# Kernel optimization log

Measured on AMD Instinct MI355X. Metric: run time of the kernel, lower is better.

The kernel has to match this reference:

```python
import jax, jax.numpy as jnp
import numpy as np

BOS, EOS, MAX_STEPS = 1, 2, 50
VOCAB, EMBD, HID, CTX, SEQ = 50257, 512, 1024, 1024, 50


def setup_inputs() -> dict:
    key = jax.random.key(0)
    ks = jax.random.split(key, 13)
    s = 0.05
    return {
        "seq_enc_states": jax.random.normal(ks[0], (SEQ, 1, CTX), jnp.float32),
        "seq_enc_hidden": jax.random.normal(ks[1], (1, CTX), jnp.float32),
        "E": jax.random.normal(ks[2], (VOCAB, EMBD), jnp.float32) * s,
        "W_init": jax.random.normal(ks[3], (HID, CTX), jnp.float32) * s,
        "b_init": jax.random.normal(ks[4], (HID,), jnp.float32) * s,
        "Wa": jax.random.normal(ks[5], (CTX, HID), jnp.float32) * s,
        "ba": jax.random.normal(ks[6], (CTX,), jnp.float32) * s,
        "W_ih": jax.random.normal(ks[7], (3 * HID, EMBD + CTX), jnp.float32) * s,
        "W_hh": jax.random.normal(ks[8], (3 * HID, HID), jnp.float32) * s,
        "b_ih": jax.random.normal(ks[9], (3 * HID,), jnp.float32) * s,
        "b_hh": jax.random.normal(ks[10], (3 * HID,), jnp.float32) * s,
        "Wv": jax.random.normal(ks[11], (VOCAB, HID), jnp.float32) * s,
        "bv": jax.random.normal(ks[12], (VOCAB,), jnp.float32) * s,
    }


def _gru_cell(x, h, W_ih, W_hh, b_ih, b_hh):
    # torch.nn.GRUCell math
    gi = x @ W_ih.T + b_ih  # (1, 3H)
    gh = h @ W_hh.T + b_hh  # (1, 3H)
    i_r, i_z, i_n = jnp.split(gi, 3, axis=-1)
    h_r, h_z, h_n = jnp.split(gh, 3, axis=-1)
    r = jax.nn.sigmoid(i_r + h_r)
    z = jax.nn.sigmoid(i_z + h_z)
    n = jnp.tanh(i_n + r * h_n)
    return (1.0 - z) * n + z * h


def reference(seq_enc_states, seq_enc_hidden, E, W_init, b_init, Wa, ba,
              W_ih, W_hh, b_ih, b_hh, Wv, bv):
    enc = seq_enc_states[:, 0, :]                       # (S, CTX)
    h0 = seq_enc_hidden.reshape(1, -1) @ W_init.T + b_init  # (1, H)
    emb0 = E[BOS][None, :]                              # (1, EMBD)

    def step(carry, _):
        h, emb, done = carry
        # dot-product attention over the 50 encoder positions
        ph = h @ Wa.T + ba                              # (1, CTX)
        attn = jax.nn.softmax(ph @ enc.T, axis=-1)      # (1, S)
        ctx = attn @ enc                                # (1, CTX)
        x = jnp.concatenate([emb, ctx], axis=-1)        # (1, EMBD+CTX)
        h_new = _gru_cell(x, h, W_ih, W_hh, b_ih, b_hh)
        logp = jax.nn.log_softmax(h_new @ Wv.T + bv, axis=-1)  # (1, V)
        idx = jnp.argmax(logp[0])
        valid = jnp.logical_not(done)
        is_eos = idx == EOS
        emit_idx = jnp.where(valid & jnp.logical_not(is_eos), idx, -1).astype(jnp.int32)
        logp_out = jnp.where(valid, logp[0], 0.0)
        new_emb = jnp.where((valid & jnp.logical_not(is_eos))[..., None], E[idx][None, :], emb)
        new_h = jnp.where(valid, h_new, h)
        new_done = done | is_eos
        return (new_h, new_emb, new_done), (emit_idx, logp_out, valid)

    init = (h0, emb0, jnp.array(False))
    _, (indices, logps, valid) = jax.lax.scan(step, init, None, length=MAX_STEPS)
    # indices: (50,) int32, -1 where past eos / eos itself (not appended in original)
    return indices, logps, valid
```

## Files before the change

kernel.cpp:

```cpp
#include <hip/hip_runtime.h>
#include <hip/hip_fp16.h>
#include <cmath>

#define VOCABSZ 50257
#define EMBD 512
#define HIDD 1024
#define CTXD 1024
#define SEQL 50
#define NSTEPS 50
#define BOS_ID 1
#define EOS_ID 2

#define NTHR 256
#define NB_GH 768
#define NB_GI 768
#define NB_WR 64
#define NB_PRE (NB_GH + NB_GI + NB_WR)
#define NB_LOG 832
#define NW_LOG (NB_LOG * 4)

#define OFF_M      0
#define OFF_T      51200
#define OFF_H      51264
#define OFF_CTX    53312
#define OFF_GI     54336
#define OFF_GH     57408
#define OFF_L      60480
#define OFF_STATS  110784
#define OFF_STATE  117440
#define OFF_WVH    117568

__device__ __forceinline__ float wred_sum(float v) {
#pragma unroll
  for (int o = 32; o > 0; o >>= 1) v += __shfl_xor(v, o, 64);
  return v;
}

__device__ __forceinline__ float dot4(float4 a, float4 b) {
  return a.x * b.x + a.y * b.y + a.z * b.z + a.w * b.w;
}

__device__ __forceinline__ float wdot1024(const float* __restrict__ row, int lane,
                                          float4 b0, float4 b1, float4 b2, float4 b3) {
  const float4* r = (const float4*)row;
  float acc = dot4(r[lane], b0) + dot4(r[lane + 64], b1) +
              dot4(r[lane + 128], b2) + dot4(r[lane + 192], b3);
  return wred_sum(acc);
}

__device__ __forceinline__ bool beats(float v, int i, float v0, int i0) {
  return v > v0 || (v == v0 && i < i0);
}

__device__ __forceinline__ void top2_merge(float& v1, int& i1, float& v2, int& i2,
                                           float w1, int j1, float w2, int j2) {
  if (beats(w1, j1, v1, i1)) {
    float nv2; int ni2;
    if (beats(v1, i1, w2, j2)) { nv2 = v1; ni2 = i1; } else { nv2 = w2; ni2 = j2; }
    v1 = w1; i1 = j1; v2 = nv2; i2 = ni2;
  } else if (beats(w1, j1, v2, i2)) {
    v2 = w1; i2 = j1;
  }
}

__device__ __forceinline__ float acc8(uint4 a, const float* b) {
  const __half2* h = reinterpret_cast<const __half2*>(&a);
  float2 f0 = __half22float2(h[0]);
  float2 f1 = __half22float2(h[1]);
  float2 f2 = __half22float2(h[2]);
  float2 f3 = __half22float2(h[3]);
  return f0.x * b[0] + f0.y * b[1] + f1.x * b[2] + f1.y * b[3] +
         f2.x * b[4] + f2.y * b[5] + f3.x * b[6] + f3.y * b[7];
}

__global__ void __launch_bounds__(NTHR)
k_cvt(const float4* __restrict__ src, uint2* __restrict__ dst, int n4) {
  int i = blockIdx.x * NTHR + threadIdx.x;
  const int stride = gridDim.x * NTHR;
  for (; i < n4; i += stride) {
    float4 v = src[i];
    __half2 a = __floats2half2_rn(v.x, v.y);
    __half2 b = __floats2half2_rn(v.z, v.w);
    uint2 u;
    u.x = *reinterpret_cast<unsigned*>(&a);
    u.y = *reinterpret_cast<unsigned*>(&b);
    dst[i] = u;
  }
}

__global__ void __launch_bounds__(1024)
k0_matM(float* __restrict__ ws, const float* __restrict__ enc,
        const float* __restrict__ Wa) {
  const int kc = blockIdx.x;
  const int jg = blockIdx.y;
  const int tid = threadIdx.x;
  const int w = tid >> 6, lane = tid & 63;
  const int jw = w & 3, q = w >> 2;
  const int j = jg * 4 + jw;
  const int k = kc * 64 + lane;
  __shared__ float s_red[16][64];
  float acc0 = 0.f, acc1 = 0.f, acc2 = 0.f, acc3 = 0.f;
  if (j < SEQL) {
    const float4* e4 = (const float4*)(enc + (size_t)j * CTXD);
    const float* Wc = Wa + k;
    for (int c4 = q * 64; c4 < q * 64 + 64; ++c4) {
      float4 e = e4[c4];
      const float* wp = Wc + (size_t)(c4 * 4) * HIDD;
      acc0 += e.x * wp[0];
      acc1 += e.y * wp[HIDD];
      acc2 += e.z * wp[2 * HIDD];
      acc3 += e.w * wp[3 * HIDD];
    }
  }
  s_red[w][lane] = acc0 + acc1 + acc2 + acc3;
  __syncthreads();
  if (q == 0 && j < SEQL) {
    float v = s_red[jw][lane] + s_red[4 + jw][lane] +
              s_red[8 + jw][lane] + s_red[12 + jw][lane];
    ws[OFF_M + (size_t)j * HIDD + k] = v;
  }
}

__global__ void __launch_bounds__(NTHR)
k0_init(float* __restrict__ ws, const float* __restrict__ enc,
        const float* __restrict__ hid0, const float* __restrict__ Winit,
        const float* __restrict__ binit, const float* __restrict__ ba) {
  const int blk = blockIdx.x, tid = threadIdx.x;
  const int wave = tid >> 6, lane = tid & 63;
  if (blk == 0) {
    const float4* b4 = (const float4*)ba;
    float4 b0 = b4[lane], b1 = b4[lane + 64], b2 = b4[lane + 128], b3 = b4[lane + 192];
    for (int j = wave; j < SEQL; j += 4) {
      float v = wdot1024(enc + (size_t)j * CTXD, lane, b0, b1, b2, b3);
      if (lane == 0) ws[OFF_T + j] = v;
    }
    if (tid == 0) {
      int* st_emb = (int*)(ws + OFF_STATE);
      st_emb[0] = BOS_ID;
      st_emb[64] = 0;
    }
  } else {
    const float4* h4 = (const float4*)hid0;
    float4 b0 = h4[lane], b1 = h4[lane + 64], b2 = h4[lane + 128], b3 = h4[lane + 192];
    int row = (blk - 1) * 4 + wave;
    float v = wdot1024(Winit + (size_t)row * CTXD, lane, b0, b1, b2, b3) + binit[row];
    if (lane == 0) ws[OFF_H + row] = v;
  }
}

__global__ void __launch_bounds__(NTHR)
k_attn0(float* __restrict__ ws, const float* __restrict__ enc) {
  const int tid = threadIdx.x;
  const int wave = tid >> 6, lane = tid & 63;
  __shared__ float s_h[HIDD];
  __shared__ float s_sc[64], s_aw[64];
  ((float4*)s_h)[tid] = ((const float4*)(ws + OFF_H))[tid];
  __syncthreads();
  const float4* h4 = (const float4*)s_h;
  float4 b0 = h4[lane], b1 = h4[lane + 64], b2 = h4[lane + 128], b3 = h4[lane + 192];
  for (int j = wave; j < SEQL; j += 4) {
    float v = wdot1024(ws + OFF_M + (size_t)j * HIDD, lane, b0, b1, b2, b3) + ws[OFF_T + j];
    if (lane == 0) s_sc[j] = v;
  }
  __syncthreads();
  if (tid < 64) {
    float v = (tid < SEQL) ? s_sc[tid] : -INFINITY;
    float mx = v;
#pragma unroll
    for (int o = 32; o > 0; o >>= 1) mx = fmaxf(mx, __shfl_xor(mx, o, 64));
    float e = (tid < SEQL) ? expf(v - mx) : 0.f;
    float sm = wred_sum(e);
    if (tid < SEQL) s_aw[tid] = e / sm;
  }
  __syncthreads();
  const float4* enc4 = (const float4*)enc;
  float4 acc = make_float4(0.f, 0.f, 0.f, 0.f);
  for (int j = 0; j < SEQL; ++j) {
    float a = s_aw[j];
    float4 ev = enc4[(size_t)j * (CTXD / 4) + tid];
    acc.x += a * ev.x; acc.y += a * ev.y; acc.z += a * ev.z; acc.w += a * ev.w;
  }
  ((float4*)(ws + OFF_CTX))[tid] = acc;
}

__global__ void __launch_bounds__(NTHR)
k_pre(float* __restrict__ ws, const float* __restrict__ E,
      const float* __restrict__ Wih, const float* __restrict__ Whh,
      const float* __restrict__ bih, const float* __restrict__ bhh,
      const float* __restrict__ Wv, const float* __restrict__ bv,
      float* __restrict__ out, int s) {
  const int blk = blockIdx.x, tid = threadIdx.x;
  const int wave = tid >> 6, lane = tid & 63;
  int* st_emb = (int*)(ws + OFF_STATE);
  int* st_done = st_emb + 64;
  const int hoff = OFF_H + (s & 1) * HIDD;

  if (blk < NB_GH) {
    if (s >= NSTEPS) return;
    const float4* h4 = (const float4*)(ws + hoff);
    float4 b0 = h4[lane], b1 = h4[lane + 64], b2 = h4[lane + 128], b3 = h4[lane + 192];
    const int r = blk * 4 + wave;
    float v = wdot1024(Whh + (size_t)r * HIDD, lane, b0, b1, b2, b3) + bhh[r];
    if (lane == 0) ws[OFF_GH + r] = v;
    return;
  }

  const bool is_writer = (blk >= NB_GH + NB_GI);
  if (!is_writer && s >= NSTEPS) return;
  if (is_writer && s == 0) return;

  int emb_s = 0, D_s = 0, gidx = -1;
  float logZ = 0.f;
  bool valid = false, eos = false;

  if (s > 0) {
    __shared__ float rm[NTHR], rs_[NTHR], rv1[NTHR], rv2[NTHR];
    __shared__ int ri1[NTHR], ri2[NTHR];
    __shared__ float s_ex[2];
    float m = -INFINITY, su = 0.f, v1 = -INFINITY, v2 = -INFINITY;
    int i1 = 0x7fffffff, i2 = 0x7fffffff;
    const float4* sb = (const float4*)(ws + OFF_STATS);
    for (int q = tid; q < NB_LOG; q += NTHR) {
      float4 A = sb[q * 2];
      float4 B = sb[q * 2 + 1];
      float mn = fmaxf(m, A.x);
      su = ((m == -INFINITY) ? 0.f : su * __expf(m - mn)) + A.y * __expf(A.x - mn);
      m = mn;
      top2_merge(v1, i1, v2, i2, A.z, __float_as_int(A.w), B.x, __float_as_int(B.y));
    }
    rm[tid] = m; rs_[tid] = su; rv1[tid] = v1; ri1[tid] = i1; rv2[tid] = v2; ri2[tid] = i2;
    __syncthreads();
    for (int st = 128; st > 0; st >>= 1) {
      if (tid < st) {
        float m2 = rm[tid + st], s2 = rs_[tid + st];
        float mn = fmaxf(rm[tid], m2);
        rs_[tid] = rs_[tid] * __expf(rm[tid] - mn) + s2 * __expf(m2 - mn);
        rm[tid] = mn;
        float a1 = rv1[tid], a2 = rv2[tid];
        int b1 = ri1[tid], b2 = ri2[tid];
        top2_merge(a1, b1, a2, b2, rv1[tid + st], ri1[tid + st], rv2[tid + st], ri2[tid + st]);
        rv1[tid] = a1; ri1[tid] = b1; rv2[tid] = a2; ri2[tid] = b2;
      }
      __syncthreads();
    }
    const int fi1 = ri1[0], fi2 = ri2[0];
    if (wave < 2) {
      const float4* h4 = (const float4*)(ws + hoff);
      float4 b0 = h4[lane], b1 = h4[lane + 64], b2 = h4[lane + 128], b3 = h4[lane + 192];
      const int r = (wave == 0) ? fi1 : fi2;
      float v = wdot1024(Wv + (size_t)r * HIDD, lane, b0, b1, b2, b3) + bv[r];
      if (lane == 0) s_ex[wave] = v;
    }
    __syncthreads();
    gidx = beats(s_ex[1], fi2, s_ex[0], fi1) ? fi2 : fi1;
    logZ = rm[0] + logf(rs_[0]);
    const int Dp = st_done[s - 1];
    valid = (Dp == 0);
    eos = (gidx == EOS_ID);
    D_s = Dp | (eos ? 1 : 0);
    emb_s = (valid && !eos) ? gidx : st_emb[s - 1];
  } else {
    emb_s = st_emb[0];
  }

  if (!is_writer) {
    const int r = (blk - NB_GH) * 4 + wave;
    const float4* e4 = (const float4*)(E + (size_t)emb_s * EMBD);
    float4 eb0 = e4[lane], eb1 = e4[lane + 64];
    const float4* c4 = (const float4*)(ws + OFF_CTX);
    float4 cb0 = c4[lane], cb1 = c4[lane + 64], cb2 = c4[lane + 128], cb3 = c4[lane + 192];
    const float* rowp = Wih + (size_t)r * (EMBD + CTXD);
    const float4* re = (const float4*)rowp;
    const float4* rc = (const float4*)(rowp + EMBD);
    float acc = dot4(re[lane], eb0) + dot4(re[lane + 64], eb1) +
                dot4(rc[lane], cb0) + dot4(rc[lane + 64], cb1) +
                dot4(rc[lane + 128], cb2) + dot4(rc[lane + 192], cb3);
    float v = wred_sum(acc) + bih[r];
    if (lane == 0) ws[OFF_GI + r] = v;
  } else {
    if (blk == NB_GH + NB_GI && tid == 0) {
      out[s - 1] = (valid && !eos) ? (float)gidx : -1.f;
      out[NSTEPS + (size_t)NSTEPS * VOCABSZ + (s - 1)] = valid ? 1.f : 0.f;
      st_emb[s] = emb_s;
      st_done[s] = D_s;
    }
    float* logp = out + NSTEPS + (size_t)(s - 1) * VOCABSZ;
    for (int i = (blk - (NB_GH + NB_GI)) * NTHR + tid; i < VOCABSZ; i += NB_WR * NTHR)
      logp[i] = valid ? (ws[OFF_L + i] - logZ) : 0.f;
  }
}

__global__ void __launch_bounds__(NTHR)
k_logits(float* __restrict__ ws, const float* __restrict__ bv,
         const float* __restrict__ enc, int s) {
  const int blk = blockIdx.x, tid = threadIdx.x;
  const int wave = tid >> 6, lane = tid & 63;
  const int p = s & 1, np = p ^ 1;
  __shared__ float s_h[HIDD];
  __shared__ float s_sc[64], s_aw[64];
  __shared__ float sm[4], ssm[4], sv1[4], sv2[4];
  __shared__ int si1[4], si2[4];

  const int* st_emb = (const int*)(ws + OFF_STATE);
  const int done = st_emb[64 + s];

  const float* hp = ws + OFF_H + p * HIDD;
#pragma unroll
  for (int it = 0; it < HIDD / NTHR; ++it) {
    const int i = tid + it * NTHR;
    float h = hp[i];
    if (done) {
      s_h[i] = h;
    } else {
      float r = 1.f / (1.f + __expf(-(ws[OFF_GI + i] + ws[OFF_GH + i])));
      float z = 1.f / (1.f + __expf(-(ws[OFF_GI + HIDD + i] + ws[OFF_GH + HIDD + i])));
      float n = tanhf(ws[OFF_GI + 2 * HIDD + i] + r * ws[OFF_GH + 2 * HIDD + i]);
      s_h[i] = (1.f - z) * n + z * h;
    }
  }
  __syncthreads();
  if (blk == 0) {
    ((float4*)(ws + OFF_H + np * HIDD))[tid] = ((const float4*)s_h)[tid];
  }

  if (blk == NB_LOG) {
    if (s + 1 < NSTEPS) {
      const float4* h4 = (const float4*)s_h;
      float4 b0 = h4[lane], b1 = h4[lane + 64], b2 = h4[lane + 128], b3 = h4[lane + 192];
      for (int j = wave; j < SEQL; j += 4) {
        float v = wdot1024(ws + OFF_M + (size_t)j * HIDD, lane, b0, b1, b2, b3) + ws[OFF_T + j];
        if (lane == 0) s_sc[j] = v;
      }
      __syncthreads();
      if (tid < 64) {
        float v = (tid < SEQL) ? s_sc[tid] : -INFINITY;
        float mx = v;
#pragma unroll
        for (int o = 32; o > 0; o >>= 1) mx = fmaxf(mx, __shfl_xor(mx, o, 64));
        float e = (tid < SEQL) ? expf(v - mx) : 0.f;
        float smv = wred_sum(e);
        if (tid < SEQL) s_aw[tid] = e / smv;
      }
      __syncthreads();
      const float4* enc4 = (const float4*)enc;
      float4 acc = make_float4(0.f, 0.f, 0.f, 0.f);
      for (int j = 0; j < SEQL; ++j) {
        float a = s_aw[j];
        float4 ev = enc4[(size_t)j * (CTXD / 4) + tid];
        acc.x += a * ev.x; acc.y += a * ev.y; acc.z += a * ev.z; acc.w += a * ev.w;
      }
      ((float4*)(ws + OFF_CTX))[tid] = acc;
    }
    return;
  }

  float hb[16];
  {
    const float4* h4 = (const float4*)s_h;
    float4 a = h4[lane * 2], b = h4[lane * 2 + 1];
    float4 c = h4[128 + lane * 2], d = h4[129 + lane * 2];
    hb[0] = a.x; hb[1] = a.y; hb[2] = a.z; hb[3] = a.w;
    hb[4] = b.x; hb[5] = b.y; hb[6] = b.z; hb[7] = b.w;
    hb[8] = c.x; hb[9] = c.y; hb[10] = c.z; hb[11] = c.w;
    hb[12] = d.x; hb[13] = d.y; hb[14] = d.z; hb[15] = d.w;
  }
  const __half* WvH = (const __half*)(ws + OFF_WVH);
  float m = -INFINITY, sum = 0.f, v1 = -INFINITY, v2 = -INFINITY;
  int i1 = 0x7fffffff, i2 = 0x7fffffff;
  for (int row = blk * 4 + wave; row < VOCABSZ; row += NW_LOG) {
    const uint4* r4 = (const uint4*)(WvH + (size_t)row * HIDD);
    float acc = acc8(r4[lane], hb) + acc8(r4[lane + 64], hb + 8);
    float l = wred_sum(acc) + bv[row];
    if (lane == 0) ws[OFF_L + row] = l;
    float mn = fmaxf(m, l);
    sum = ((m == -INFINITY) ? 0.f : sum * __expf(m - mn)) + __expf(l - mn);
    m = mn;
    if (beats(l, row, v1, i1)) { v2 = v1; i2 = i1; v1 = l; i1 = row; }
    else if (beats(l, row, v2, i2)) { v2 = l; i2 = row; }
  }
  if (lane == 0) {
    sm[wave] = m; ssm[wave] = sum;
    sv1[wave] = v1; si1[wave] = i1; sv2[wave] = v2; si2[wave] = i2;
  }
  __syncthreads();
  if (tid == 0) {
    float mm = sm[0], su = ssm[0], a1 = sv1[0], a2 = sv2[0];
    int b1 = si1[0], b2 = si2[0];
#pragma unroll
    for (int w = 1; w < 4; ++w) {
      float mn = fmaxf(mm, sm[w]);
      su = su * __expf(mm - mn) + ssm[w] * __expf(sm[w] - mn);
      mm = mn;
      top2_merge(a1, b1, a2, b2, sv1[w], si1[w], sv2[w], si2[w]);
    }
    float* st = ws + OFF_STATS + (size_t)blk * 8;
    st[0] = mm; st[1] = su;
    st[2] = a1; st[3] = __int_as_float(b1);
    st[4] = a2; st[5] = __int_as_float(b2);
  }
}

extern "C" void kernel_launch(void* const* d_in, const int* in_sizes, int n_in,
                              void* d_out, int out_size, void* d_ws, size_t ws_size,
                              hipStream_t stream) {
  const float* enc   = (const float*)d_in[0];
  const float* hid0  = (const float*)d_in[1];
  const float* E     = (const float*)d_in[2];
  const float* Winit = (const float*)d_in[3];
  const float* binit = (const float*)d_in[4];
  const float* Wa    = (const float*)d_in[5];
  const float* ba    = (const float*)d_in[6];
  const float* Wih   = (const float*)d_in[7];
  const float* Whh   = (const float*)d_in[8];
  const float* bih   = (const float*)d_in[9];
  const float* bhh   = (const float*)d_in[10];
  const float* Wv    = (const float*)d_in[11];
  const float* bv    = (const float*)d_in[12];
  float* out = (float*)d_out;
  float* ws  = (float*)d_ws;

  const int n4 = (VOCABSZ * HIDD) / 4;
  k_cvt<<<4096, NTHR, 0, stream>>>((const float4*)Wv, (uint2*)(ws + OFF_WVH), n4);
  k0_matM<<<dim3(16, 13), 1024, 0, stream>>>(ws, enc, Wa);
  k0_init<<<257, NTHR, 0, stream>>>(ws, enc, hid0, Winit, binit, ba);
  k_attn0<<<1, NTHR, 0, stream>>>(ws, enc);
  for (int s = 0; s < NSTEPS; ++s) {
    k_pre<<<NB_PRE, NTHR, 0, stream>>>(ws, E, Wih, Whh, bih, bhh, Wv, bv, out, s);
    k_logits<<<NB_LOG + 1, NTHR, 0, stream>>>(ws, bv, enc, s);
  }
  k_pre<<<NB_PRE, NTHR, 0, stream>>>(ws, E, Wih, Whh, bih, bhh, Wv, bv, out, NSTEPS);
}
```

Baseline: 1.840 ms.

## Move W_hh gate matvec from k_pre into k_logits alongside vocab projection

The hidden-to-hidden GRU gate matvec (gh = W_hh·h + b_hh) for the next step is now computed by extra blocks in k_logits, right after the new hidden state is formed. It no longer runs as 768 blocks in k_pre. A new init kernel computes the first step's gh together with the initial attention. This shortens the latency-critical k_pre, which sits between the argmax reduction and the W_ih matvec, by overlapping the W_hh work with the large vocab projection. The trade-off is that k_logits now carries extra blocks, each doing four rows per wave.

```diff
diff --git a/kernel.cpp b/kernel.cpp
--- a/kernel.cpp
+++ b/kernel.cpp
@@ -12,12 +12,12 @@
 #define EOS_ID 2
 
 #define NTHR 256
-#define NB_GH 768
 #define NB_GI 768
 #define NB_WR 64
-#define NB_PRE (NB_GH + NB_GI + NB_WR)
+#define NB_PRE (NB_GI + NB_WR)
 #define NB_LOG 832
 #define NW_LOG (NB_LOG * 4)
+#define NB_GHN 192
 
 #define OFF_M      0
 #define OFF_T      51200
@@ -148,13 +148,11 @@
   }
 }
 
-__global__ void __launch_bounds__(NTHR)
-k_attn0(float* __restrict__ ws, const float* __restrict__ enc) {
-  const int tid = threadIdx.x;
-  const int wave = tid >> 6, lane = tid & 63;
-  __shared__ float s_h[HIDD];
-  __shared__ float s_sc[64], s_aw[64];
-  ((float4*)s_h)[tid] = ((const float4*)(ws + OFF_H))[tid];
+__device__ __forceinline__ void attn_from(float* __restrict__ ws, int hoff,
+                                          const float* __restrict__ enc,
+                                          int tid, int wave, int lane,
+                                          float* s_h, float* s_sc, float* s_aw) {
+  ((float4*)s_h)[tid] = ((const float4*)(ws + hoff))[tid];
   __syncthreads();
   const float4* h4 = (const float4*)s_h;
   float4 b0 = h4[lane], b1 = h4[lane + 64], b2 = h4[lane + 128], b3 = h4[lane + 192];
@@ -184,9 +182,26 @@
 }
 
 __global__ void __launch_bounds__(NTHR)
+k_init2(float* __restrict__ ws, const float* __restrict__ enc,
+        const float* __restrict__ Whh, const float* __restrict__ bhh) {
+  const int blk = blockIdx.x, tid = threadIdx.x;
+  const int wave = tid >> 6, lane = tid & 63;
+  if (blk == 0) {
+    __shared__ float s_h[HIDD];
+    __shared__ float s_sc[64], s_aw[64];
+    attn_from(ws, OFF_H, enc, tid, wave, lane, s_h, s_sc, s_aw);
+  } else {
+    const float4* h4 = (const float4*)(ws + OFF_H);
+    float4 b0 = h4[lane], b1 = h4[lane + 64], b2 = h4[lane + 128], b3 = h4[lane + 192];
+    const int r = (blk - 1) * 4 + wave;
+    float v = wdot1024(Whh + (size_t)r * HIDD, lane, b0, b1, b2, b3) + bhh[r];
+    if (lane == 0) ws[OFF_GH + r] = v;
+  }
+}
+
+__global__ void __launch_bounds__(NTHR)
 k_pre(float* __restrict__ ws, const float* __restrict__ E,
-      const float* __restrict__ Wih, const float* __restrict__ Whh,
-      const float* __restrict__ bih, const float* __restrict__ bhh,
+      const float* __restrict__ Wih, const float* __restrict__ bih,
       const float* __restrict__ Wv, const float* __restrict__ bv,
       float* __restrict__ out, int s) {
   const int blk = blockIdx.x, tid = threadIdx.x;
@@ -195,17 +210,7 @@
   int* st_done = st_emb + 64;
   const int hoff = OFF_H + (s & 1) * HIDD;
 
-  if (blk < NB_GH) {
-    if (s >= NSTEPS) return;
-    const float4* h4 = (const float4*)(ws + hoff);
-    float4 b0 = h4[lane], b1 = h4[lane + 64], b2 = h4[lane + 128], b3 = h4[lane + 192];
-    const int r = blk * 4 + wave;
-    float v = wdot1024(Whh + (size_t)r * HIDD, lane, b0, b1, b2, b3) + bhh[r];
-    if (lane == 0) ws[OFF_GH + r] = v;
-    return;
-  }
-
-  const bool is_writer = (blk >= NB_GH + NB_GI);
+  const bool is_writer = (blk >= NB_GI);
   if (!is_writer && s >= NSTEPS) return;
   if (is_writer && s == 0) return;
 
@@ -264,7 +269,7 @@
   }
 
   if (!is_writer) {
-    const int r = (blk - NB_GH) * 4 + wave;
+    const int r = blk * 4 + wave;
     const float4* e4 = (const float4*)(E + (size_t)emb_s * EMBD);
     float4 eb0 = e4[lane], eb1 = e4[lane + 64];
     const float4* c4 = (const float4*)(ws + OFF_CTX);
@@ -278,28 +283,26 @@
     float v = wred_sum(acc) + bih[r];
     if (lane == 0) ws[OFF_GI + r] = v;
   } else {
-    if (blk == NB_GH + NB_GI && tid == 0) {
+    if (blk == NB_GI && tid == 0) {
       out[s - 1] = (valid && !eos) ? (float)gidx : -1.f;
       out[NSTEPS + (size_t)NSTEPS * VOCABSZ + (s - 1)] = valid ? 1.f : 0.f;
       st_emb[s] = emb_s;
       st_done[s] = D_s;
     }
     float* logp = out + NSTEPS + (size_t)(s - 1) * VOCABSZ;
-    for (int i = (blk - (NB_GH + NB_GI)) * NTHR + tid; i < VOCABSZ; i += NB_WR * NTHR)
+    for (int i = (blk - NB_GI) * NTHR + tid; i < VOCABSZ; i += NB_WR * NTHR)
       logp[i] = valid ? (ws[OFF_L + i] - logZ) : 0.f;
   }
 }
 
 __global__ void __launch_bounds__(NTHR)
 k_logits(float* __restrict__ ws, const float* __restrict__ bv,
-         const float* __restrict__ enc, int s) {
+         const float* __restrict__ enc, const float* __restrict__ Whh,
+         const float* __restrict__ bhh, int s) {
   const int blk = blockIdx.x, tid = threadIdx.x;
   const int wave = tid >> 6, lane = tid & 63;
   const int p = s & 1, np = p ^ 1;
   __shared__ float s_h[HIDD];
-  __shared__ float s_sc[64], s_aw[64];
-  __shared__ float sm[4], ssm[4], sv1[4], sv2[4];
-  __shared__ int si1[4], si2[4];
 
   const int* st_emb = (const int*)(ws + OFF_STATE);
   const int done = st_emb[64 + s];
@@ -323,8 +326,23 @@
     ((float4*)(ws + OFF_H + np * HIDD))[tid] = ((const float4*)s_h)[tid];
   }
 
+  if (blk > NB_LOG) {
+    if (s + 1 >= NSTEPS) return;
+    const float4* h4 = (const float4*)s_h;
+    float4 b0 = h4[lane], b1 = h4[lane + 64], b2 = h4[lane + 128], b3 = h4[lane + 192];
+    const int wid = (blk - NB_LOG - 1) * 4 + wave;
+#pragma unroll
+    for (int k = 0; k < 4; ++k) {
+      const int r = wid + 768 * k;
+      float v = wdot1024(Whh + (size_t)r * HIDD, lane, b0, b1, b2, b3) + bhh[r];
+      if (lane == 0) ws[OFF_GH + r] = v;
+    }
+    return;
+  }
+
   if (blk == NB_LOG) {
     if (s + 1 < NSTEPS) {
+      __shared__ float s_sc[64], s_aw[64];
       const float4* h4 = (const float4*)s_h;
       float4 b0 = h4[lane], b1 = h4[lane + 64], b2 = h4[lane + 128], b3 = h4[lane + 192];
       for (int j = wave; j < SEQL; j += 4) {
@@ -354,6 +372,8 @@
     return;
   }
 
+  __shared__ float sm[4], ssm[4], sv1[4], sv2[4];
+  __shared__ int si1[4], si2[4];
   float hb[16];
   {
     const float4* h4 = (const float4*)s_h;
@@ -423,10 +443,10 @@
   k_cvt<<<4096, NTHR, 0, stream>>>((const float4*)Wv, (uint2*)(ws + OFF_WVH), n4);
   k0_matM<<<dim3(16, 13), 1024, 0, stream>>>(ws, enc, Wa);
   k0_init<<<257, NTHR, 0, stream>>>(ws, enc, hid0, Winit, binit, ba);
-  k_attn0<<<1, NTHR, 0, stream>>>(ws, enc);
+  k_init2<<<769, NTHR, 0, stream>>>(ws, enc, Whh, bhh);
   for (int s = 0; s < NSTEPS; ++s) {
-    k_pre<<<NB_PRE, NTHR, 0, stream>>>(ws, E, Wih, Whh, bih, bhh, Wv, bv, out, s);
-    k_logits<<<NB_LOG + 1, NTHR, 0, stream>>>(ws, bv, enc, s);
-  }
-  k_pre<<<NB_PRE, NTHR, 0, stream>>>(ws, E, Wih, Whh, bih, bhh, Wv, bv, out, NSTEPS);
-}
+    k_pre<<<NB_PRE, NTHR, 0, stream>>>(ws, E, Wih, bih, Wv, bv, out, s);
+    k_logits<<<NB_LOG + 1 + NB_GHN, NTHR, 0, stream>>>(ws, bv, enc, Whh, bhh, s);
+  }
+  k_pre<<<NB_PRE, NTHR, 0, stream>>>(ws, E, Wih, bih, Wv, bv, out, NSTEPS);
+}
```

Measured after the change: 1.836 ms. About the same (-0.2%).
